# Kernel tuning notes

Hardware: AMD Instinct MI355X
Metric: run time of the kernel (lower is better)

Reference implementation:

```python
import jax, jax.numpy as jnp
import numpy as np

H = 512  # hidden_dim


def setup_inputs() -> dict:
    key = jax.random.key(0)
    ks = jax.random.split(key, 13)
    s = 0.05  # weight scale to keep sigmoid/tanh out of saturation
    inp = {
        "inputs": jax.random.normal(ks[0], (256, 256, 512), jnp.float32),  # [T,B,D]
        "enc_w1": jax.random.normal(ks[1], (512, 128), jnp.float32) * s,
        "enc_b1": jax.random.normal(ks[2], (128,), jnp.float32) * s,
        "enc_w2": jax.random.normal(ks[3], (128, 64), jnp.float32) * s,
        "enc_b2": jax.random.normal(ks[4], (64,), jnp.float32) * s,
        "enc_w3": jax.random.normal(ks[5], (64, 512), jnp.float32) * s,
        "enc_b3": jax.random.normal(ks[6], (512,), jnp.float32) * s,
        "gate_w": jax.random.normal(ks[7], (1024, 4 * H), jnp.float32) * s,  # [D+H, 4H] order f,i,g,o
        "gate_b": jax.random.normal(ks[8], (4 * H,), jnp.float32) * s,
        "samp_w1": jax.random.normal(ks[9], (4, 8), jnp.float32) * s,
        "samp_b1": jax.random.normal(ks[10], (8,), jnp.float32) * s,
        "samp_w2": jax.random.normal(ks[11], (8, 4), jnp.float32) * s,
        "samp_b2": jax.random.normal(ks[12], (4,), jnp.float32) * s,
    }
    return inp


def reference(inputs, enc_w1, enc_b1, enc_w2, enc_b2, enc_w3, enc_b3,
              gate_w, gate_b, samp_w1, samp_b1, samp_w2, samp_b2):
    T, B, D = inputs.shape
    # Sampler mask is computed on a constant ones(1,4), so it is value-invariant
    # across timesteps: hoist out of the loop (identical math).
    ones4 = jnp.ones((1, 4), inputs.dtype)
    mask = jax.nn.softmax(jnp.tanh(ones4 @ samp_w1 + samp_b1) @ samp_w2 + samp_b2, axis=-1)[0]  # [4]

    def step(carry, x):  # x: [B, D]
        hx, cx = carry
        # autoencoder encode: D -> 128 -> 64 -> latent(=D); dropout is identity at eval
        h1 = jax.nn.relu(x @ enc_w1 + enc_b1)
        h2 = jax.nn.relu(h1 @ enc_w2 + enc_b2)
        comp = h2 @ enc_w3 + enc_b3                      # [B, latent]
        combined = jnp.concatenate([comp, hx], axis=1)   # [B, latent+H]
        gates = combined @ gate_w + gate_b               # fused 4-gate GEMM [B, 4H]
        f, i, g, o = jnp.split(gates, 4, axis=1)
        f = jax.nn.sigmoid(f) * mask[0]
        i = jax.nn.sigmoid(i) * mask[1]
        g = jnp.tanh(g) * mask[2]
        o = jax.nn.sigmoid(o) * mask[3]
        cx = f * cx + i * g
        hx = o * jnp.tanh(cx)
        return (hx, cx), hx

    hx0 = jnp.zeros((B, H), inputs.dtype)
    cx0 = jnp.zeros((B, H), inputs.dtype)
    (hx, cx), stacked = jax.lax.scan(step, (hx0, cx0), inputs)
    return stacked, hx, cx
```

## Files before the change

kernel.cpp:

```cpp
#include <hip/hip_runtime.h>
#include <hip/hip_bf16.h>

typedef __attribute__((ext_vector_type(8))) short short8;
typedef __attribute__((ext_vector_type(4))) float float4v;
typedef __attribute__((ext_vector_type(2))) float float2v;

#define T_STEPS 256
#define BATCH   256
#define DIM     512
#define HID     512

__device__ __forceinline__ float bf2f(unsigned short u) {
  unsigned int v = ((unsigned int)u) << 16;
  union { unsigned int i; float f; } c; c.i = v; return c.f;
}
__device__ __forceinline__ unsigned short f2bf(float f) {
  union { float f; unsigned int i; } c; c.f = f;
  unsigned int x = c.i;
  x += 0x7fffu + ((x >> 16) & 1u);
  return (unsigned short)(x >> 16);
}
__device__ __forceinline__ float sigm(float x) {
  return __builtin_amdgcn_rcpf(1.0f + __expf(-x));
}
__device__ __forceinline__ float tanh_(float x) {
  return 1.0f - 2.0f * __builtin_amdgcn_rcpf(1.0f + __expf(2.0f * x));
}

template<bool RELU, bool A_F32>
__global__ void enc_gemm(const void* __restrict__ Av,
                         const float* __restrict__ Bw,
                         const float* __restrict__ bias,
                         unsigned short* __restrict__ C,
                         int M, int N, int K) {
  const int tid  = threadIdx.x;
  const int lane = tid & 63;
  const int r = lane & 15, q = lane >> 4;
  const int waveId = blockIdx.x * 4 + (tid >> 6);
  const int nT = N >> 5;
  const int m0 = (waveId / nT) << 5;
  const int n0 = (waveId % nT) << 5;
  float4v acc[2][2] = {};
  const int ks = K >> 5;
  for (int s = 0; s < ks; ++s) {
    short8 a[2], b[2];
#pragma unroll
    for (int mt = 0; mt < 2; ++mt) {
      const size_t off = (size_t)(m0 + mt * 16 + r) * K + s * 32 + q * 8;
      if (A_F32) {
        const float* A = (const float*)Av;
        const float4v lo = *(const float4v*)(A + off);
        const float4v hi = *(const float4v*)(A + off + 4);
        short8 f;
#pragma unroll
        for (int j = 0; j < 4; ++j) { f[j] = (short)f2bf(lo[j]); f[j + 4] = (short)f2bf(hi[j]); }
        a[mt] = f;
      } else {
        a[mt] = *(const short8*)((const unsigned short*)Av + off);
      }
    }
#pragma unroll
    for (int nt = 0; nt < 2; ++nt) {
      const int col = n0 + nt * 16 + r;
      short8 f;
#pragma unroll
      for (int j = 0; j < 8; ++j)
        f[j] = (short)f2bf(Bw[(size_t)(s * 32 + q * 8 + j) * N + col]);
      b[nt] = f;
    }
#pragma unroll
    for (int mt = 0; mt < 2; ++mt)
#pragma unroll
      for (int nt = 0; nt < 2; ++nt)
        acc[mt][nt] = __builtin_amdgcn_mfma_f32_16x16x32_bf16(a[mt], b[nt], acc[mt][nt], 0, 0, 0);
  }
#pragma unroll
  for (int nt = 0; nt < 2; ++nt) {
    const float bv = bias[n0 + nt * 16 + r];
#pragma unroll
    for (int mt = 0; mt < 2; ++mt)
#pragma unroll
      for (int i = 0; i < 4; ++i) {
        float v = acc[mt][nt][i] + bv;
        if (RELU) v = fmaxf(v, 0.0f);
        C[(size_t)(m0 + mt * 16 + q * 4 + i) * N + n0 + nt * 16 + r] = f2bf(v);
      }
  }
}

__global__ __launch_bounds__(256, 1) void qlstm_rec(
    const unsigned short* __restrict__ comp,
    const float* __restrict__ gw,
    const float* __restrict__ gb,
    const float* __restrict__ sw1, const float* __restrict__ sb1,
    const float* __restrict__ sw2, const float* __restrict__ sb2,
    unsigned short* __restrict__ hxbuf,
    unsigned int* __restrict__ bar,
    float* __restrict__ out)
{
  __shared__ float lds_g[4][32][68];
  const int tid  = threadIdx.x;
  const int lane = tid & 63;
  const int wv   = tid >> 6;
  const int r = lane & 15, q = lane >> 4;
  const int gid  = blockIdx.x & 7;
  const int rank = blockIdx.x >> 3;
  const int b0 = gid << 5;
  const int h0 = rank << 4;

  float t1[8];
#pragma unroll
  for (int j = 0; j < 8; ++j) {
    float s = sb1[j];
#pragma unroll
    for (int k = 0; k < 4; ++k) s += sw1[k * 8 + j];
    t1[j] = tanhf(s);
  }
  float s2[4];
#pragma unroll
  for (int c = 0; c < 4; ++c) {
    float s = sb2[c];
#pragma unroll
    for (int j = 0; j < 8; ++j) s += t1[j] * sw2[j * 4 + c];
    s2[c] = s;
  }
  const float mx = fmaxf(fmaxf(s2[0], s2[1]), fmaxf(s2[2], s2[3]));
  const float e0 = __expf(s2[0] - mx), e1 = __expf(s2[1] - mx);
  const float e2 = __expf(s2[2] - mx), e3 = __expf(s2[3] - mx);
  const float inv = 1.0f / (e0 + e1 + e2 + e3);
  const float m0f = e0 * inv, m1f = e1 * inv, m2f = e2 * inv, m3f = e3 * inv;

  short8 Bf[4][8];
  const int kbase = wv << 8;
#pragma unroll
  for (int nt = 0; nt < 4; ++nt) {
    const int col = nt * 512 + h0 + r;
#pragma unroll
    for (int s = 0; s < 8; ++s) {
      short8 f;
      const int kk = kbase + s * 32 + q * 8;
#pragma unroll
      for (int j = 0; j < 8; ++j)
        f[j] = (short)f2bf(gw[(size_t)(kk + j) * 2048 + col]);
      Bf[nt][s] = f;
    }
  }

  const int bl = tid & 31;
  const int hp = tid >> 5;
  float bias_v[2][4];
#pragma unroll
  for (int u = 0; u < 2; ++u)
#pragma unroll
    for (int gt = 0; gt < 4; ++gt)
      bias_v[u][gt] = gb[gt * 512 + h0 + 2 * hp + u];
  float cxv[2] = {0.0f, 0.0f};
  float2v hx_last = {0.0f, 0.0f};

  const unsigned short* hx0p = hxbuf;
  const unsigned short* hx1p = hxbuf + BATCH * HID;
  unsigned int* barp = bar + gid * 16;

  short8 aC[2][8], aN[2][8];
  if (wv < 2) {
#pragma unroll
    for (int s = 0; s < 8; ++s)
#pragma unroll
      for (int mt = 0; mt < 2; ++mt)
        aC[mt][s] = *(const short8*)(comp + (size_t)(b0 + mt * 16 + r) * DIM + kbase + s * 32 + q * 8);
  }

  auto step = [&](int t, short8 (&acur)[2][8], short8 (&anext)[2][8]) {
    const unsigned short* hxr = (t & 1) ? hx1p : hx0p;
    unsigned short* hxw = (unsigned short*)((t & 1) ? hx0p : hx1p);
    if (wv >= 2) {
#pragma unroll
      for (int s = 0; s < 8; ++s)
#pragma unroll
        for (int mt = 0; mt < 2; ++mt) {
          const unsigned long long* p = (const unsigned long long*)(hxr +
              (size_t)(b0 + mt * 16 + r) * HID + (wv - 2) * 256 + s * 32 + q * 8);
          union { unsigned long long u[2]; short8 s8; } x;
          x.u[0] = __hip_atomic_load((unsigned long long*)p,     __ATOMIC_RELAXED, __HIP_MEMORY_SCOPE_AGENT);
          x.u[1] = __hip_atomic_load((unsigned long long*)p + 1, __ATOMIC_RELAXED, __HIP_MEMORY_SCOPE_AGENT);
          acur[mt][s] = x.s8;
        }
    }
    float4v acc[2][4] = {};
#pragma unroll
    for (int s = 0; s < 8; ++s)
#pragma unroll
      for (int mt = 0; mt < 2; ++mt)
#pragma unroll
        for (int nt = 0; nt < 4; ++nt)
          acc[mt][nt] = __builtin_amdgcn_mfma_f32_16x16x32_bf16(acur[mt][s], Bf[nt][s], acc[mt][nt], 0, 0, 0);
#pragma unroll
    for (int mt = 0; mt < 2; ++mt)
#pragma unroll
      for (int nt = 0; nt < 4; ++nt)
#pragma unroll
        for (int i = 0; i < 4; ++i)
          lds_g[wv][mt * 16 + q * 4 + i][nt * 16 + r] = acc[mt][nt][i];
    __syncthreads();
    float ga[2][4];
#pragma unroll
    for (int u = 0; u < 2; ++u)
#pragma unroll
      for (int gt = 0; gt < 4; ++gt) ga[u][gt] = bias_v[u][gt];
#pragma unroll
    for (int w = 0; w < 4; ++w)
#pragma unroll
      for (int gt = 0; gt < 4; ++gt) {
        const float2v pr = *(const float2v*)&lds_g[w][bl][gt * 16 + 2 * hp];
        ga[0][gt] += pr[0]; ga[1][gt] += pr[1];
      }
    float hxf[2];
#pragma unroll
    for (int u = 0; u < 2; ++u) {
      const float f = sigm(ga[u][0]) * m0f;
      const float i = sigm(ga[u][1]) * m1f;
      const float g = tanh_(ga[u][2]) * m2f;
      const float o = sigm(ga[u][3]) * m3f;
      const float c = f * cxv[u] + i * g;
      cxv[u] = c;
      hxf[u] = o * tanh_(c);
    }
    hx_last[0] = hxf[0]; hx_last[1] = hxf[1];
    const unsigned int hx_pack = (unsigned int)f2bf(hxf[0]) | ((unsigned int)f2bf(hxf[1]) << 16);
    const int hcol = h0 + 2 * hp;
    __hip_atomic_store((unsigned int*)(hxw + (size_t)(b0 + bl) * HID + hcol), hx_pack,
                       __ATOMIC_RELAXED, __HIP_MEMORY_SCOPE_AGENT);
    *(float2v*)(out + (size_t)(t * BATCH + b0 + bl) * HID + hcol) = hx_last;
    asm volatile("" ::: "memory");
    if (wv < 2) {
      const int tn = (t < T_STEPS - 1) ? (t + 1) : t;
#pragma unroll
      for (int s = 0; s < 8; ++s)
#pragma unroll
        for (int mt = 0; mt < 2; ++mt)
          anext[mt][s] = *(const short8*)(comp + (size_t)(tn * BATCH + b0 + mt * 16 + r) * DIM + kbase + s * 32 + q * 8);
    }
    __syncthreads();
    if (t < T_STEPS - 1) {
      if (tid == 192) {
        __hip_atomic_fetch_add(barp, 1u, __ATOMIC_RELAXED, __HIP_MEMORY_SCOPE_AGENT);
        const unsigned int tgt = 32u * (unsigned int)(t + 1);
        while (__hip_atomic_load(barp, __ATOMIC_RELAXED, __HIP_MEMORY_SCOPE_AGENT) < tgt)
          __builtin_amdgcn_s_sleep(2);
      }
      __syncthreads();
    }
  };

#pragma unroll 1
  for (int t = 0; t < T_STEPS; t += 2) {
    step(t, aC, aN);
    step(t + 1, aN, aC);
  }

  const int hcol = h0 + 2 * hp;
  const size_t base = (size_t)T_STEPS * BATCH * HID;
  *(float2v*)(out + base + (size_t)(b0 + bl) * HID + hcol) = hx_last;
  float2v cxo = {cxv[0], cxv[1]};
  *(float2v*)(out + base + (size_t)BATCH * HID + (size_t)(b0 + bl) * HID + hcol) = cxo;
}

extern "C" void kernel_launch(void* const* d_in, const int* in_sizes, int n_in,
                              void* d_out, int out_size, void* d_ws, size_t ws_size,
                              hipStream_t stream) {
  const float* x   = (const float*)d_in[0];
  const float* w1  = (const float*)d_in[1];
  const float* b1  = (const float*)d_in[2];
  const float* w2  = (const float*)d_in[3];
  const float* b2  = (const float*)d_in[4];
  const float* w3  = (const float*)d_in[5];
  const float* b3  = (const float*)d_in[6];
  const float* gw  = (const float*)d_in[7];
  const float* gb  = (const float*)d_in[8];
  const float* sw1 = (const float*)d_in[9];
  const float* sb1 = (const float*)d_in[10];
  const float* sw2 = (const float*)d_in[11];
  const float* sb2 = (const float*)d_in[12];
  float* out = (float*)d_out;

  char* ws = (char*)d_ws;
  unsigned short* comp = (unsigned short*)ws;
  unsigned short* hxb  = (unsigned short*)(ws + (size_t)67108864);
  unsigned int*   bar  = (unsigned int*)(ws + (size_t)67108864 + 524288);
  unsigned short* h1 = (unsigned short*)d_out;
  unsigned short* h2 = h1 + (size_t)65536 * 128;

  hipMemsetAsync(hxb, 0, (size_t)BATCH * HID * 2, stream);
  hipMemsetAsync(bar, 0, 512, stream);

  enc_gemm<true , true ><<<dim3(2048), 256, 0, stream>>>(x,  w1, b1, h1,   65536, 128, 512);
  enc_gemm<true , false><<<dim3(1024), 256, 0, stream>>>(h1, w2, b2, h2,   65536,  64, 128);
  enc_gemm<false, false><<<dim3(8192), 256, 0, stream>>>(h2, w3, b3, comp, 65536, 512,  64);

  qlstm_rec<<<dim3(256), 256, 0, stream>>>(comp, gw, gb, sw1, sb1, sw2, sb2, hxb, bar, out);
}
```

Baseline: 1.605 ms.

## Overlap comp-side MFMA with grid barrier by per-wave arrival and hx-wave spin

Replaces the block-level grid barrier (one thread arrives and spins, then __syncthreads) with a per-wave arrival counter: every wave increments the counter after draining its stores, and only the hx-reading waves spin on it before loading the recurrent state. The comp-input waves now prefetch the next timestep and run their MFMA half without waiting on the barrier, so the input-projection work overlaps the inter-block synchronisation. This drops one __syncthreads per step. In exchange the hx waves busy-spin without sleep and the counter target grows to 128 per step, which raises atomic traffic on the barrier word.

After: 2.377 ms. +48.1%, slower.

```diff
diff --git a/kernel.cpp b/kernel.cpp
--- a/kernel.cpp
+++ b/kernel.cpp
@@ -161,6 +161,10 @@
   const unsigned short* hx1p = hxbuf + BATCH * HID;
   unsigned int* barp = bar + gid * 16;
 
+  const int colb = ((wv >= 2) ? (wv - 2) : 0) * 256 + q * 8;
+  const size_t hxoff0 = (size_t)(b0 + r) * HID + colb;
+  const size_t hxoff1 = hxoff0 + (size_t)16 * HID;
+
   short8 aC[2][8], aN[2][8];
   if (wv < 2) {
 #pragma unroll
@@ -173,27 +177,49 @@
   auto step = [&](int t, short8 (&acur)[2][8], short8 (&anext)[2][8]) {
     const unsigned short* hxr = (t & 1) ? hx1p : hx0p;
     unsigned short* hxw = (unsigned short*)((t & 1) ? hx0p : hx1p);
-    if (wv >= 2) {
+    float4v acc[2][4] = {};
+    if (wv < 2) {
+      const int tn = (t < T_STEPS - 1) ? (t + 1) : t;
 #pragma unroll
       for (int s = 0; s < 8; ++s)
 #pragma unroll
-        for (int mt = 0; mt < 2; ++mt) {
-          const unsigned long long* p = (const unsigned long long*)(hxr +
-              (size_t)(b0 + mt * 16 + r) * HID + (wv - 2) * 256 + s * 32 + q * 8);
+        for (int mt = 0; mt < 2; ++mt)
+          anext[mt][s] = *(const short8*)(comp + (size_t)(tn * BATCH + b0 + mt * 16 + r) * DIM + kbase + s * 32 + q * 8);
+#pragma unroll
+      for (int s = 0; s < 8; ++s)
+#pragma unroll
+        for (int mt = 0; mt < 2; ++mt)
+#pragma unroll
+          for (int nt = 0; nt < 4; ++nt)
+            acc[mt][nt] = __builtin_amdgcn_mfma_f32_16x16x32_bf16(acur[mt][s], Bf[nt][s], acc[mt][nt], 0, 0, 0);
+    } else {
+      const unsigned int tgt = 128u * (unsigned int)t;
+      while (__hip_atomic_load(barp, __ATOMIC_RELAXED, __HIP_MEMORY_SCOPE_AGENT) < tgt) {}
+#pragma unroll
+      for (int s = 0; s < 8; ++s) {
+        {
+          const unsigned long long* p = (const unsigned long long*)(hxr + hxoff0 + s * 32);
           union { unsigned long long u[2]; short8 s8; } x;
           x.u[0] = __hip_atomic_load((unsigned long long*)p,     __ATOMIC_RELAXED, __HIP_MEMORY_SCOPE_AGENT);
           x.u[1] = __hip_atomic_load((unsigned long long*)p + 1, __ATOMIC_RELAXED, __HIP_MEMORY_SCOPE_AGENT);
-          acur[mt][s] = x.s8;
+          acur[0][s] = x.s8;
         }
-    }
-    float4v acc[2][4] = {};
-#pragma unroll
-    for (int s = 0; s < 8; ++s)
-#pragma unroll
-      for (int mt = 0; mt < 2; ++mt)
-#pragma unroll
-        for (int nt = 0; nt < 4; ++nt)
-          acc[mt][nt] = __builtin_amdgcn_mfma_f32_16x16x32_bf16(acur[mt][s], Bf[nt][s], acc[mt][nt], 0, 0, 0);
+        {
+          const unsigned long long* p = (const unsigned long long*)(hxr + hxoff1 + s * 32);
+          union { unsigned long long u[2]; short8 s8; } x;
+          x.u[0] = __hip_atomic_load((unsigned long long*)p,     __ATOMIC_RELAXED, __HIP_MEMORY_SCOPE_AGENT);
+          x.u[1] = __hip_atomic_load((unsigned long long*)p + 1, __ATOMIC_RELAXED, __HIP_MEMORY_SCOPE_AGENT);
+          acur[1][s] = x.s8;
+        }
+      }
+#pragma unroll
+      for (int s = 0; s < 8; ++s)
+#pragma unroll
+        for (int mt = 0; mt < 2; ++mt)
+#pragma unroll
+          for (int nt = 0; nt < 4; ++nt)
+            acc[mt][nt] = __builtin_amdgcn_mfma_f32_16x16x32_bf16(acur[mt][s], Bf[nt][s], acc[mt][nt], 0, 0, 0);
+    }
 #pragma unroll
     for (int mt = 0; mt < 2; ++mt)
 #pragma unroll
@@ -231,25 +257,10 @@
     __hip_atomic_store((unsigned int*)(hxw + (size_t)(b0 + bl) * HID + hcol), hx_pack,
                        __ATOMIC_RELAXED, __HIP_MEMORY_SCOPE_AGENT);
     *(float2v*)(out + (size_t)(t * BATCH + b0 + bl) * HID + hcol) = hx_last;
-    asm volatile("" ::: "memory");
-    if (wv < 2) {
-      const int tn = (t < T_STEPS - 1) ? (t + 1) : t;
-#pragma unroll
-      for (int s = 0; s < 8; ++s)
-#pragma unroll
-        for (int mt = 0; mt < 2; ++mt)
-          anext[mt][s] = *(const short8*)(comp + (size_t)(tn * BATCH + b0 + mt * 16 + r) * DIM + kbase + s * 32 + q * 8);
-    }
+    asm volatile("s_waitcnt vmcnt(0)" ::: "memory");
+    if ((t < T_STEPS - 1) && lane == 0)
+      __hip_atomic_fetch_add(barp, 1u, __ATOMIC_RELAXED, __HIP_MEMORY_SCOPE_AGENT);
     __syncthreads();
-    if (t < T_STEPS - 1) {
-      if (tid == 192) {
-        __hip_atomic_fetch_add(barp, 1u, __ATOMIC_RELAXED, __HIP_MEMORY_SCOPE_AGENT);
-        const unsigned int tgt = 32u * (unsigned int)(t + 1);
-        while (__hip_atomic_load(barp, __ATOMIC_RELAXED, __HIP_MEMORY_SCOPE_AGENT) < tgt)
-          __builtin_amdgcn_s_sleep(2);
-      }
-      __syncthreads();
-    }
   };
 
 #pragma unroll 1
```
